# Kernel tuning notes

Measured on AMD Instinct MI355X. Metric: run time of the kernel, lower is better.

Reference implementation:

```python
import jax, jax.numpy as jnp
import numpy as np

ALPHA = float(np.exp(-0.1))  # leak factor exp(-dt/tau) with dt/tau = 0.1


def setup_inputs() -> dict:
    key = jax.random.key(0)
    k1, k2 = jax.random.split(key)
    B, T, H, O = 128, 512, 1024, 256
    x = jax.random.normal(k1, (B, T, H), dtype=jnp.float32)
    # xavier_uniform init for (H, O) weight
    limit = float(np.sqrt(6.0 / (H + O)))
    weight_end = jax.random.uniform(k2, (H, O), dtype=jnp.float32,
                                    minval=-limit, maxval=limit)
    return {"x": x, "weight_end": weight_end}


def reference(x, weight_end):
    # x: [B, T, H], weight_end: [H, O]
    h2 = jnp.einsum('bth,ho->bto', x, weight_end)  # [B, T, O]
    B, T, O = h2.shape
    # leaky-integrate scan over first T-1 steps, accumulating softmax(mem)
    h_seq = jnp.swapaxes(h2[:, :T - 1, :], 0, 1)  # [T-1, B, O]

    def step(carry, h_t):
        mem, out = carry
        mem = ALPHA * mem + (1.0 - ALPHA) * h_t
        out = out + jax.nn.softmax(mem, axis=-1)
        return (mem, out), None

    init = (jnp.zeros((B, O), h2.dtype), jnp.zeros((B, O), h2.dtype))
    (_, out), _ = jax.lax.scan(step, init, h_seq)
    return out
```

## Files before the change

kernel.cpp:

```cpp
#include <hip/hip_runtime.h>

#define B_DIM 128
#define T_DIM 512
#define H_DIM 1024
#define O_DIM 256

typedef short bf16x8 __attribute__((ext_vector_type(8)));
typedef float f32x4 __attribute__((ext_vector_type(4)));

__device__ __forceinline__ unsigned short f2bf(float f) {
    union { float f; unsigned u; } v; v.f = f;
    unsigned u = v.u;
    u += 0x7fffu + ((u >> 16) & 1u);
    return (unsigned short)(u >> 16);
}

__device__ __forceinline__ unsigned tpk(float a, float b) {
    union { float f; unsigned u; } x{a}, y{b};
    return __builtin_amdgcn_perm(y.u, x.u, 0x07060302u);
}

__device__ __forceinline__ void async16(const void* g, void* l) {
    __builtin_amdgcn_global_load_lds(
        (const __attribute__((address_space(1))) unsigned int*)g,
        (__attribute__((address_space(3))) unsigned int*)l, 16, 0, 0);
}

__global__ __launch_bounds__(256) void transpose_w(const float* __restrict__ W,
                                                   unsigned short* __restrict__ Wt) {
    __shared__ float tile[32][33];
    int h0 = blockIdx.x * 32;
    int o0 = blockIdx.y * 32;
    int tx = threadIdx.x;
    int ty = threadIdx.y;
#pragma unroll
    for (int j = 0; j < 32; j += 8)
        tile[ty + j][tx] = W[(size_t)(h0 + ty + j) * O_DIM + o0 + tx];
    __syncthreads();
    int h = h0 + tx;
#pragma unroll
    for (int j = 0; j < 32; j += 8) {
        int o = o0 + ty + j;
        size_t idx = (size_t)(o >> 7) * 131072 + (size_t)(h >> 5) * 4096 +
                     (size_t)((h >> 3) & 3) * 1024 + (size_t)(o & 127) * 8 + (h & 7);
        Wt[idx] = f2bf(tile[tx][ty + j]);
    }
}

__global__ __launch_bounds__(256, 4) void gemm_bf16(const float* __restrict__ x,
                                                    const unsigned short* __restrict__ Wtt,
                                                    unsigned short* __restrict__ h2) {
    __shared__ __align__(16) unsigned short As[2][128 * 40];
    __shared__ __align__(16) unsigned short Bs[2][4096];

    const int tid  = threadIdx.x;
    const int mb   = blockIdx.x >> 1;
    const int nb   = blockIdx.x & 1;
    const int m0   = mb * 128, n0 = nb * 128;
    const int lane = tid & 63;
    const int wave = tid >> 6;
    const int wm   = wave >> 1, wn = wave & 1;
    const int rowsel = lane & 15, quad = lane >> 4;

    const int arow = wave * 32 + (lane >> 3);
    const int akf  = (lane & 7) * 4;
    const float* ag = x + (size_t)(m0 + arow) * H_DIM + akf;
    const int aoff = arow * 40 + akf;

    const unsigned short* bg = Wtt + (size_t)nb * 131072 + (size_t)tid * 8;
    unsigned short* bl0 = (unsigned short*)&Bs[0][tid * 8];
    unsigned short* bl1 = (unsigned short*)&Bs[1][tid * 8];

    f32x4 acc[4][4];
#pragma unroll
    for (int i = 0; i < 4; ++i)
#pragma unroll
        for (int j = 0; j < 4; ++j)
            acc[i][j] = (f32x4){0.f, 0.f, 0.f, 0.f};

    {
        float4 a[4];
#pragma unroll
        for (int i = 0; i < 4; ++i)
            a[i] = *(const float4*)(ag + (size_t)i * 8 * H_DIM);
        async16(bg, bl0);
        async16(bg + 2048, bl0 + 2048);
#pragma unroll
        for (int i = 0; i < 4; ++i) {
            uint2 p;
            p.x = tpk(a[i].x, a[i].y);
            p.y = tpk(a[i].z, a[i].w);
            *(uint2*)&As[0][aoff + i * 8 * 40] = p;
        }
    }

    for (int k = 0; k < 32; ++k) {
        const int cur = k & 1, nxt = cur ^ 1;
        __syncthreads();

        float4 a[4];
        if (k + 1 < 32) {
            const float* agk = ag + (size_t)(k + 1) * 32;
#pragma unroll
            for (int i = 0; i < 4; ++i)
                a[i] = *(const float4*)(agk + (size_t)i * 8 * H_DIM);
            const unsigned short* bgk = bg + (size_t)(k + 1) * 4096;
            unsigned short* bl = nxt ? bl1 : bl0;
            async16(bgk, bl);
            async16(bgk + 2048, bl + 2048);
        }

        bf16x8 af[4], bfr[4];
#pragma unroll
        for (int i = 0; i < 4; ++i) {
            af[i]  = *(const bf16x8*)&As[cur][(wm * 64 + rowsel + i * 16) * 40 + quad * 8];
            bfr[i] = *(const bf16x8*)&Bs[cur][quad * 1024 + (wn * 64 + rowsel + i * 16) * 8];
        }
#pragma unroll
        for (int i = 0; i < 4; ++i)
#pragma unroll
            for (int j = 0; j < 4; ++j)
                acc[i][j] = __builtin_amdgcn_mfma_f32_16x16x32_bf16(af[i], bfr[j], acc[i][j], 0, 0, 0);

        if (k + 1 < 32) {
#pragma unroll
            for (int i = 0; i < 4; ++i) {
                uint2 p;
                p.x = tpk(a[i].x, a[i].y);
                p.y = tpk(a[i].z, a[i].w);
                *(uint2*)&As[nxt][aoff + i * 8 * 40] = p;
            }
        }
    }

#pragma unroll
    for (int i = 0; i < 4; ++i) {
#pragma unroll
        for (int j = 0; j < 4; ++j) {
            int gm = m0 + wm * 64 + i * 16 + quad * 4;
            int gn = n0 + wn * 64 + j * 16 + rowsel;
            unsigned short* cp = h2 + (size_t)gm * O_DIM + gn;
            cp[0 * O_DIM] = f2bf(acc[i][j][0]);
            cp[1 * O_DIM] = f2bf(acc[i][j][1]);
            cp[2 * O_DIM] = f2bf(acc[i][j][2]);
            cp[3 * O_DIM] = f2bf(acc[i][j][3]);
        }
    }
}

__global__ __launch_bounds__(64) void snn_scan(const unsigned short* __restrict__ h2,
                                               float* __restrict__ out) {
    const int b = blockIdx.x >> 3;
    const int c = blockIdx.x & 7;
    const int t_start = c * 64;
    const int t_end   = min(t_start + 64, T_DIM - 1);
    const int s0      = max(0, t_start - 64);
    const int lane    = threadIdx.x;

    const float A   = 0.90483741803595957f;
    const float OMA = 0.09516258196404043f;

    const unsigned short* base = h2 + (size_t)b * T_DIM * O_DIM + lane * 4;
#define LD(row) (*(const uint2*)(base + (size_t)(row) * O_DIM))

    float4 mem = {0.f, 0.f, 0.f, 0.f};
    float4 acc = {0.f, 0.f, 0.f, 0.f};

    uint2 u0 = LD(s0), u1 = LD(s0 + 1), u2 = LD(s0 + 2), u3 = LD(s0 + 3);

    const int nIter = (t_end - s0 + 3) & ~3;

#define STEP(U, T)                                                              \
    {                                                                           \
        union { unsigned u; float f; } l0, h0, l1, h1;                          \
        l0.u = (U).x << 16; h0.u = (U).x & 0xffff0000u;                         \
        l1.u = (U).y << 16; h1.u = (U).y & 0xffff0000u;                         \
        mem.x = A * mem.x + OMA * l0.f;                                         \
        mem.y = A * mem.y + OMA * h0.f;                                         \
        mem.z = A * mem.z + OMA * l1.f;                                         \
        mem.w = A * mem.w + OMA * h1.f;                                         \
        if ((T) >= t_start && (T) < t_end) {                                    \
            float e0 = __expf(mem.x), e1 = __expf(mem.y);                       \
            float e2 = __expf(mem.z), e3 = __expf(mem.w);                       \
            float s = e0 + e1 + e2 + e3;                                        \
            s += __shfl_xor(s, 1);                                              \
            s += __shfl_xor(s, 2);                                              \
            s += __shfl_xor(s, 4);                                              \
            s += __shfl_xor(s, 8);                                              \
            s += __shfl_xor(s, 16);                                             \
            s += __shfl_xor(s, 32);                                             \
            float inv = 1.0f / s;                                               \
            acc.x += e0 * inv; acc.y += e1 * inv;                               \
            acc.z += e2 * inv; acc.w += e3 * inv;                               \
        }                                                                       \
    }

    for (int t = s0; t < s0 + nIter; t += 4) {
        STEP(u0, t);     u0 = LD(min(t + 4, T_DIM - 1));
        STEP(u1, t + 1); u1 = LD(min(t + 5, T_DIM - 1));
        STEP(u2, t + 2); u2 = LD(min(t + 6, T_DIM - 1));
        STEP(u3, t + 3); u3 = LD(min(t + 7, T_DIM - 1));
    }
#undef STEP
#undef LD

    float* op = out + b * O_DIM + lane * 4;
    atomicAdd(op + 0, acc.x);
    atomicAdd(op + 1, acc.y);
    atomicAdd(op + 2, acc.z);
    atomicAdd(op + 3, acc.w);
}

extern "C" void kernel_launch(void* const* d_in, const int* in_sizes, int n_in,
                              void* d_out, int out_size, void* d_ws, size_t ws_size,
                              hipStream_t stream) {
    const float* x = (const float*)d_in[0];
    const float* W = (const float*)d_in[1];
    float* out = (float*)d_out;

    unsigned short* h2 = (unsigned short*)d_ws;
    unsigned short* Wt = (unsigned short*)((char*)d_ws +
                         (size_t)B_DIM * T_DIM * O_DIM * sizeof(unsigned short));

    hipMemsetAsync(d_out, 0, (size_t)B_DIM * O_DIM * sizeof(float), stream);
    transpose_w<<<dim3(H_DIM / 32, O_DIM / 32), dim3(32, 8), 0, stream>>>(W, Wt);
    gemm_bf16<<<dim3((B_DIM * T_DIM / 128) * 2), 256, 0, stream>>>(x, Wt, h2);
    snn_scan<<<dim3(B_DIM * 8), 64, 0, stream>>>(h2, out);
}
```

Measured before the change: 444.1 us.

## Widen GEMM block to cover all output columns so x is read once

The GEMM now uses 512-thread blocks with 8 waves, and each block computes a 128x256 tile spanning the full output width instead of two 128x128 blocks per row tile. The fp32 input x, the largest tensor, is therefore loaded from global memory once instead of twice. The cost is a larger B buffer in shared memory and more threads per block, which may reduce occupancy.

```diff
diff --git a/kernel.cpp b/kernel.cpp
--- a/kernel.cpp
+++ b/kernel.cpp
@@ -47,29 +47,27 @@
     }
 }
 
-__global__ __launch_bounds__(256, 4) void gemm_bf16(const float* __restrict__ x,
+__global__ __launch_bounds__(512, 4) void gemm_bf16(const float* __restrict__ x,
                                                     const unsigned short* __restrict__ Wtt,
                                                     unsigned short* __restrict__ h2) {
     __shared__ __align__(16) unsigned short As[2][128 * 40];
-    __shared__ __align__(16) unsigned short Bs[2][4096];
+    __shared__ __align__(16) unsigned short Bs[2][8192];
 
     const int tid  = threadIdx.x;
-    const int mb   = blockIdx.x >> 1;
-    const int nb   = blockIdx.x & 1;
-    const int m0   = mb * 128, n0 = nb * 128;
+    const int mb   = blockIdx.x;
+    const int m0   = mb * 128;
     const int lane = tid & 63;
     const int wave = tid >> 6;
-    const int wm   = wave >> 1, wn = wave & 1;
+    const int wm   = wave >> 2, wn = wave & 3;
     const int rowsel = lane & 15, quad = lane >> 4;
 
-    const int arow = wave * 32 + (lane >> 3);
-    const int akf  = (lane & 7) * 4;
+    const int arow = tid >> 3;
+    const int akf  = (tid & 7) * 4;
     const float* ag = x + (size_t)(m0 + arow) * H_DIM + akf;
     const int aoff = arow * 40 + akf;
 
-    const unsigned short* bg = Wtt + (size_t)nb * 131072 + (size_t)tid * 8;
-    unsigned short* bl0 = (unsigned short*)&Bs[0][tid * 8];
-    unsigned short* bl1 = (unsigned short*)&Bs[1][tid * 8];
+    const unsigned short* bg0 = Wtt + (size_t)tid * 8;
+    const unsigned short* bg1 = Wtt + 131072 + (size_t)tid * 8;
 
     f32x4 acc[4][4];
 #pragma unroll
@@ -79,42 +77,42 @@
             acc[i][j] = (f32x4){0.f, 0.f, 0.f, 0.f};
 
     {
-        float4 a[4];
-#pragma unroll
-        for (int i = 0; i < 4; ++i)
-            a[i] = *(const float4*)(ag + (size_t)i * 8 * H_DIM);
-        async16(bg, bl0);
-        async16(bg + 2048, bl0 + 2048);
-#pragma unroll
-        for (int i = 0; i < 4; ++i) {
-            uint2 p;
-            p.x = tpk(a[i].x, a[i].y);
-            p.y = tpk(a[i].z, a[i].w);
-            *(uint2*)&As[0][aoff + i * 8 * 40] = p;
-        }
-    }
+        float4 a0 = *(const float4*)(ag);
+        float4 a1 = *(const float4*)(ag + (size_t)64 * H_DIM);
+        unsigned short* bl = &Bs[0][tid * 8];
+        async16(bg0, bl);
+        async16(bg1, bl + 4096);
+        uint2 p0, p1;
+        p0.x = tpk(a0.x, a0.y); p0.y = tpk(a0.z, a0.w);
+        p1.x = tpk(a1.x, a1.y); p1.y = tpk(a1.z, a1.w);
+        *(uint2*)&As[0][aoff] = p0;
+        *(uint2*)&As[0][aoff + 64 * 40] = p1;
+    }
+
+    const int nbsel = wn >> 1;
+    const int bbase = nbsel * 4096 + quad * 1024;
+    const int bcol0 = (wn & 1) * 64 + rowsel;
 
     for (int k = 0; k < 32; ++k) {
         const int cur = k & 1, nxt = cur ^ 1;
         __syncthreads();
 
-        float4 a[4];
+        float4 a0, a1;
         if (k + 1 < 32) {
             const float* agk = ag + (size_t)(k + 1) * 32;
-#pragma unroll
-            for (int i = 0; i < 4; ++i)
-                a[i] = *(const float4*)(agk + (size_t)i * 8 * H_DIM);
-            const unsigned short* bgk = bg + (size_t)(k + 1) * 4096;
-            unsigned short* bl = nxt ? bl1 : bl0;
-            async16(bgk, bl);
-            async16(bgk + 2048, bl + 2048);
+            a0 = *(const float4*)(agk);
+            a1 = *(const float4*)(agk + (size_t)64 * H_DIM);
+            const size_t bko = (size_t)(k + 1) * 4096;
+            unsigned short* bl = &Bs[nxt][tid * 8];
+            async16(bg0 + bko, bl);
+            async16(bg1 + bko, bl + 4096);
         }
 
         bf16x8 af[4], bfr[4];
 #pragma unroll
         for (int i = 0; i < 4; ++i) {
             af[i]  = *(const bf16x8*)&As[cur][(wm * 64 + rowsel + i * 16) * 40 + quad * 8];
-            bfr[i] = *(const bf16x8*)&Bs[cur][quad * 1024 + (wn * 64 + rowsel + i * 16) * 8];
+            bfr[i] = *(const bf16x8*)&Bs[cur][bbase + (bcol0 + i * 16) * 8];
         }
 #pragma unroll
         for (int i = 0; i < 4; ++i)
@@ -123,13 +121,11 @@
                 acc[i][j] = __builtin_amdgcn_mfma_f32_16x16x32_bf16(af[i], bfr[j], acc[i][j], 0, 0, 0);
 
         if (k + 1 < 32) {
-#pragma unroll
-            for (int i = 0; i < 4; ++i) {
-                uint2 p;
-                p.x = tpk(a[i].x, a[i].y);
-                p.y = tpk(a[i].z, a[i].w);
-                *(uint2*)&As[nxt][aoff + i * 8 * 40] = p;
-            }
+            uint2 p0, p1;
+            p0.x = tpk(a0.x, a0.y); p0.y = tpk(a0.z, a0.w);
+            p1.x = tpk(a1.x, a1.y); p1.y = tpk(a1.z, a1.w);
+            *(uint2*)&As[nxt][aoff] = p0;
+            *(uint2*)&As[nxt][aoff + 64 * 40] = p1;
         }
     }
 
@@ -138,7 +134,7 @@
 #pragma unroll
         for (int j = 0; j < 4; ++j) {
             int gm = m0 + wm * 64 + i * 16 + quad * 4;
-            int gn = n0 + wn * 64 + j * 16 + rowsel;
+            int gn = wn * 64 + j * 16 + rowsel;
             unsigned short* cp = h2 + (size_t)gm * O_DIM + gn;
             cp[0 * O_DIM] = f2bf(acc[i][j][0]);
             cp[1 * O_DIM] = f2bf(acc[i][j][1]);
@@ -224,6 +220,6 @@
 
     hipMemsetAsync(d_out, 0, (size_t)B_DIM * O_DIM * sizeof(float), stream);
     transpose_w<<<dim3(H_DIM / 32, O_DIM / 32), dim3(32, 8), 0, stream>>>(W, Wt);
-    gemm_bf16<<<dim3((B_DIM * T_DIM / 128) * 2), 256, 0, stream>>>(x, Wt, h2);
+    gemm_bf16<<<dim3(B_DIM * T_DIM / 128), 512, 0, stream>>>(x, Wt, h2);
     snn_scan<<<dim3(B_DIM * 8), 64, 0, stream>>>(h2, out);
 }
```

After: 433.5 us. -2.4%, faster.
